# Performance work log

Measured on AMD Instinct MI355X. Metric: run time of the kernel, lower is better.

The kernel has to match this reference:

```python
import jax, jax.numpy as jnp
import numpy as np

K = 16          # top-k per pooled row
EPS = 1e-12     # tf.nn.l2_normalize epsilon


def setup_inputs() -> dict:
    key = jax.random.key(0)
    x = jax.random.normal(key, (16, 256, 128, 128), dtype=jnp.float32)
    return {"x": x}


def reference(x) -> tuple:
    # x: [B, C, H, W]; last_n_dims = 2 -> pool the trailing H*W axis.
    B, C, H, W = x.shape
    flat = x.reshape(B, C, H * W)                       # [B, C, HW]
    # tf.nn.l2_normalize(axis=-1): x / sqrt(max(sum(x^2), eps))
    sq = jnp.sum(flat * flat, axis=-1, keepdims=True)
    normed = flat * jax.lax.rsqrt(jnp.maximum(sq, EPS))  # [B, C, HW]
    top_k_value, top_k_idx = jax.lax.top_k(normed, K)    # [B, C, K]
    # decode flat indices into (h, w) coordinates (div/mod loop in original)
    h = top_k_idx // W
    w = top_k_idx % W
    coors = jnp.stack([h, w], axis=-1).astype(jnp.int32)  # [B, C, K, 2]
    return top_k_value, coors
```

## Files before the change

### kernel.cpp

```cpp
#include <hip/hip_runtime.h>


#define KSEL 16
#define HW   16384
#define WDIM 128
#define CAP  1024
#define T0   2.5f
#define NROWS 4096
#define VALS_TOTAL (NROWS * KSEL)

typedef float floatx4 __attribute__((ext_vector_type(4)));

__global__ __launch_bounds__(256) void k_fused(const float* __restrict__ x,
                                               float* __restrict__ out) {
    const int row  = blockIdx.x;
    const int t    = threadIdx.x;
    const int lane = t & 63;
    const int wv   = t >> 6;

    __shared__ unsigned long long s_cand[CAP];
    __shared__ float s_part[4][4];
    __shared__ unsigned s_cnt;

    if (t == 0) s_cnt = 0;
    __syncthreads();

    const floatx4* p = (const floatx4*)(x + (size_t)row * HW);

    float sqsum[4];
    #pragma unroll
    for (int c = 0; c < 4; ++c) {
        floatx4 buf[4];
        #pragma unroll
        for (int k = 0; k < 4; ++k)
            buf[k] = __builtin_nontemporal_load(&p[c * 1024 + k * 256 + t]);

        float s = 0.0f;
        #pragma unroll
        for (int k = 0; k < 4; ++k) {
            s = fmaf(buf[k].x, buf[k].x, s);
            s = fmaf(buf[k].y, buf[k].y, s);
            s = fmaf(buf[k].z, buf[k].z, s);
            s = fmaf(buf[k].w, buf[k].w, s);
        }
        sqsum[c] = s;

        unsigned msk = 0;
        #pragma unroll
        for (int k = 0; k < 4; ++k) {
            msk |= (buf[k].x > T0) ? (1u << (4 * k + 0)) : 0u;
            msk |= (buf[k].y > T0) ? (1u << (4 * k + 1)) : 0u;
            msk |= (buf[k].z > T0) ? (1u << (4 * k + 2)) : 0u;
            msk |= (buf[k].w > T0) ? (1u << (4 * k + 3)) : 0u;
        }
        if (msk) {
            unsigned base = atomicAdd(&s_cnt, (unsigned)__popc(msk));
            #pragma unroll
            for (int k = 0; k < 4; ++k) {
                #pragma unroll
                for (int cc = 0; cc < 4; ++cc) {
                    float v = (cc == 0) ? buf[k].x : (cc == 1) ? buf[k].y
                            : (cc == 2) ? buf[k].z : buf[k].w;
                    if (v > T0) {
                        if (base < CAP) {
                            unsigned u  = __float_as_uint(v);
                            unsigned mm = u ^ (((unsigned)((int)u >> 31)) | 0x80000000u);
                            int idx = c * 4096 + (k * 256 + t) * 4 + cc;
                            s_cand[base] = ((unsigned long long)mm << 32) |
                                           (unsigned)(16383 - idx);
                        }
                        base++;
                    }
                }
            }
        }
    }

    #pragma unroll
    for (int c = 0; c < 4; ++c) {
        float s = sqsum[c];
        #pragma unroll
        for (int off = 32; off > 0; off >>= 1)
            s += __shfl_down(s, off, 64);
        if (lane == 0) s_part[c][wv] = s;
    }
    __syncthreads();

    const float q0 = s_part[0][0] + s_part[0][1] + s_part[0][2] + s_part[0][3];
    const float q1 = s_part[1][0] + s_part[1][1] + s_part[1][2] + s_part[1][3];
    const float q2 = s_part[2][0] + s_part[2][1] + s_part[2][2] + s_part[2][3];
    const float q3 = s_part[3][0] + s_part[3][1] + s_part[3][2] + s_part[3][3];
    const float scale = 1.0f / sqrtf(fmaxf(q0 + q1 + q2 + q3, 1e-12f));

    unsigned cnt = s_cnt;

    if (cnt < KSEL || cnt > CAP) {
        const float* xr = x + (size_t)row * HW;
        float T = T0, lo = -3.0e38f, hi = 3.0e38f;
        for (int it = 0; it < 32; ++it) {
            __syncthreads();
            if (t == 0) s_cnt = 0;
            __syncthreads();
            for (int i = t; i < HW; i += 256) {
                float v = xr[i];
                if (v > T) {
                    unsigned slot = atomicAdd(&s_cnt, 1u);
                    if (slot < CAP) {
                        unsigned u  = __float_as_uint(v);
                        unsigned mm = u ^ (((unsigned)((int)u >> 31)) | 0x80000000u);
                        s_cand[slot] = ((unsigned long long)mm << 32) |
                                       (unsigned)(16383 - i);
                    }
                }
            }
            __syncthreads();
            cnt = s_cnt;
            if (cnt >= KSEL && cnt <= CAP) break;
            if (cnt < KSEL) { hi = T; T = (lo < -1.0e38f) ? T - 1.0f : 0.5f * (lo + T); }
            else            { lo = T; T = (hi >  1.0e38f) ? T + 1.0f : 0.5f * (T + hi); }
        }
        if (cnt > CAP) cnt = CAP;
    }

    for (unsigned i = t; i < cnt; i += 256) {
        unsigned long long pk = s_cand[i];
        unsigned m = (unsigned)(pk >> 32);
        unsigned u = (m & 0x80000000u) ? (m ^ 0x80000000u) : ~m;
        float vn = __uint_as_float(u) * scale;
        unsigned u2 = __float_as_uint(vn);
        unsigned m2 = u2 ^ (((unsigned)((int)u2 >> 31)) | 0x80000000u);
        s_cand[i] = ((unsigned long long)m2 << 32) | (pk & 0xFFFFFFFFull);
    }
    __syncthreads();

    for (unsigned i = t; i < cnt; i += 256) {
        unsigned long long pk = s_cand[i];
        int rank = 0;
        for (unsigned j = 0; j < cnt; ++j) rank += (s_cand[j] > pk) ? 1 : 0;
        if (rank < KSEL) {
            unsigned m = (unsigned)(pk >> 32);
            unsigned u = (m & 0x80000000u) ? (m ^ 0x80000000u) : ~m;
            float vn = __uint_as_float(u);
            int idx = 16383 - (int)(unsigned)(pk & 0xFFFFFFFFull);
            out[row * KSEL + rank] = vn;
            float* coor = out + VALS_TOTAL + ((size_t)row * KSEL + rank) * 2;
            coor[0] = (float)(idx >> 7);
            coor[1] = (float)(idx & (WDIM - 1));
        }
    }
}

extern "C" void kernel_launch(void* const* d_in, const int* in_sizes, int n_in,
                              void* d_out, int out_size, void* d_ws, size_t ws_size,
                              hipStream_t stream) {
    const float* x = (const float*)d_in[0];
    float* out = (float*)d_out;
    (void)d_ws; (void)ws_size;
    k_fused<<<NROWS, 256, 0, stream>>>(x, out);
}
```

Before: 330.7 us.

## Process each row with a single wavefront using double-buffered loads

Shrinks each row's block from four wavefronts to one 64-lane wavefront that walks all sixteen chunks of the row. It double-buffers the nontemporal vector loads so the next chunk is in flight while the current one is processed. The cross-wave shared-memory reduction is replaced by wave shuffles and a broadcast of the scale. This removes block-level sync and shared partial sums, but each wave now has four times the serial work and fewer bytes in flight per block, so it relies on more resident blocks per CU to keep memory bandwidth saturated.

```diff
diff --git a/kernel.cpp b/kernel.cpp
--- a/kernel.cpp
+++ b/kernel.cpp
@@ -11,30 +11,22 @@
 
 typedef float floatx4 __attribute__((ext_vector_type(4)));
 
-__global__ __launch_bounds__(256) void k_fused(const float* __restrict__ x,
-                                               float* __restrict__ out) {
-    const int row  = blockIdx.x;
-    const int t    = threadIdx.x;
-    const int lane = t & 63;
-    const int wv   = t >> 6;
+__global__ __launch_bounds__(64) void k_fused(const float* __restrict__ x,
+                                              float* __restrict__ out) {
+    const int row = blockIdx.x;
+    const int l   = threadIdx.x;
 
     __shared__ unsigned long long s_cand[CAP];
-    __shared__ float s_part[4][4];
     __shared__ unsigned s_cnt;
 
-    if (t == 0) s_cnt = 0;
+    if (l == 0) s_cnt = 0;
     __syncthreads();
 
     const floatx4* p = (const floatx4*)(x + (size_t)row * HW);
 
-    float sqsum[4];
-    #pragma unroll
-    for (int c = 0; c < 4; ++c) {
-        floatx4 buf[4];
-        #pragma unroll
-        for (int k = 0; k < 4; ++k)
-            buf[k] = __builtin_nontemporal_load(&p[c * 1024 + k * 256 + t]);
+    float q[4] = {0.0f, 0.0f, 0.0f, 0.0f};
 
+    auto process = [&](const floatx4* buf, int c, int w) {
         float s = 0.0f;
         #pragma unroll
         for (int k = 0; k < 4; ++k) {
@@ -43,7 +35,6 @@
             s = fmaf(buf[k].z, buf[k].z, s);
             s = fmaf(buf[k].w, buf[k].w, s);
         }
-        sqsum[c] = s;
 
         unsigned msk = 0;
         #pragma unroll
@@ -65,7 +56,7 @@
                         if (base < CAP) {
                             unsigned u  = __float_as_uint(v);
                             unsigned mm = u ^ (((unsigned)((int)u >> 31)) | 0x80000000u);
-                            int idx = c * 4096 + (k * 256 + t) * 4 + cc;
+                            int idx = c * 4096 + (k * 256 + w * 64 + l) * 4 + cc;
                             s_cand[base] = ((unsigned long long)mm << 32) |
                                            (unsigned)(16383 - idx);
                         }
@@ -74,24 +65,38 @@
                 }
             }
         }
-    }
 
-    #pragma unroll
-    for (int c = 0; c < 4; ++c) {
-        float s = sqsum[c];
         #pragma unroll
         for (int off = 32; off > 0; off >>= 1)
             s += __shfl_down(s, off, 64);
-        if (lane == 0) s_part[c][wv] = s;
+        if (l == 0) q[c] += s;
+    };
+
+    floatx4 bufA[4], bufB[4];
+    #pragma unroll
+    for (int k = 0; k < 4; ++k)
+        bufA[k] = __builtin_nontemporal_load(&p[k * 256 + l]);
+    #pragma unroll
+    for (int u = 0; u < 16; ++u) {
+        const int c = u >> 2, w = u & 3;
+        if (u < 15) {
+            const int cn = (u + 1) >> 2, wn = (u + 1) & 3;
+            floatx4* nxt = (u & 1) ? bufA : bufB;
+            #pragma unroll
+            for (int k = 0; k < 4; ++k)
+                nxt[k] = __builtin_nontemporal_load(
+                    &p[cn * 1024 + k * 256 + wn * 64 + l]);
+            process((u & 1) ? bufB : bufA, c, w);
+        } else {
+            process((u & 1) ? bufB : bufA, c, w);
+        }
     }
+
+    float total = ((q[0] + q[1]) + q[2]) + q[3];
+    float scale = 1.0f / sqrtf(fmaxf(total, 1e-12f));
+    scale = __shfl(scale, 0, 64);
+
     __syncthreads();
-
-    const float q0 = s_part[0][0] + s_part[0][1] + s_part[0][2] + s_part[0][3];
-    const float q1 = s_part[1][0] + s_part[1][1] + s_part[1][2] + s_part[1][3];
-    const float q2 = s_part[2][0] + s_part[2][1] + s_part[2][2] + s_part[2][3];
-    const float q3 = s_part[3][0] + s_part[3][1] + s_part[3][2] + s_part[3][3];
-    const float scale = 1.0f / sqrtf(fmaxf(q0 + q1 + q2 + q3, 1e-12f));
-
     unsigned cnt = s_cnt;
 
     if (cnt < KSEL || cnt > CAP) {
@@ -99,9 +104,9 @@
         float T = T0, lo = -3.0e38f, hi = 3.0e38f;
         for (int it = 0; it < 32; ++it) {
             __syncthreads();
-            if (t == 0) s_cnt = 0;
+            if (l == 0) s_cnt = 0;
             __syncthreads();
-            for (int i = t; i < HW; i += 256) {
+            for (int i = l; i < HW; i += 64) {
                 float v = xr[i];
                 if (v > T) {
                     unsigned slot = atomicAdd(&s_cnt, 1u);
@@ -122,7 +127,7 @@
         if (cnt > CAP) cnt = CAP;
     }
 
-    for (unsigned i = t; i < cnt; i += 256) {
+    for (unsigned i = l; i < cnt; i += 64) {
         unsigned long long pk = s_cand[i];
         unsigned m = (unsigned)(pk >> 32);
         unsigned u = (m & 0x80000000u) ? (m ^ 0x80000000u) : ~m;
@@ -133,7 +138,7 @@
     }
     __syncthreads();
 
-    for (unsigned i = t; i < cnt; i += 256) {
+    for (unsigned i = l; i < cnt; i += 64) {
         unsigned long long pk = s_cand[i];
         int rank = 0;
         for (unsigned j = 0; j < cnt; ++j) rank += (s_cand[j] > pk) ? 1 : 0;
@@ -156,5 +161,5 @@
     const float* x = (const float*)d_in[0];
     float* out = (float*)d_out;
     (void)d_ws; (void)ws_size;
-    k_fused<<<NROWS, 256, 0, stream>>>(x, out);
+    k_fused<<<NROWS, 64, 0, stream>>>(x, out);
 }
```

Measured after the change: 338.0 us. 2.2% more time.
